# Kernel optimization log

Hardware: AMD Instinct MI355X
Metric: run time of the kernel (lower is better)

## Reference

```python
import jax, jax.numpy as jnp
import numpy as np

NH = 16        # hidden buckets
NG = 32        # static attrs
NR = 16        # routing lags
HS = 256       # MLP hidden size
RHO_WARMUP = 639


def _mlp(x, W1, b1, W2, b2):
    # eval mode: dropout disabled
    return jnp.tanh(x @ W1 + b1) @ W2 + b2


def setup_inputs() -> dict:
    key = jax.random.key(0)
    ks = jax.random.split(key, 16)
    nt, ns = 1000, 500
    x = jax.random.normal(ks[0], (nt, ns, 6), dtype=jnp.float32)
    xc = jax.random.normal(ks[1], (ns, NG), dtype=jnp.float32)

    def lin(k, fan_in, fan_out):
        kw, kb = jax.random.split(k)
        s = 1.0 / np.sqrt(fan_in)
        W = jax.random.uniform(kw, (fan_in, fan_out), jnp.float32, -s, s)
        b = jax.random.uniform(kb, (fan_out,), jnp.float32, -s, s)
        return W, b

    Wr1, br1 = lin(ks[2], NG, HS)
    Wr2, br2 = lin(ks[3], HS, NH * NR)
    Ww1, bw1 = lin(ks[4], NG, HS)
    Ww2, bw2 = lin(ks[5], HS, NH * 7)
    Wt1, bt1 = lin(ks[6], 6 + NG, HS)
    Wt2, bt2 = lin(ks[7], HS, NH * 3)
    return dict(x=x, xc=xc, Wr1=Wr1, br1=br1, Wr2=Wr2, br2=br2,
                Ww1=Ww1, bw1=bw1, Ww2=Ww2, bw2=bw2,
                Wt1=Wt1, bt1=bt1, Wt2=Wt2, bt2=bt2)


def _forward(x, xc, Wr1, br1, Wr2, br2, Ww1, bw1, Ww2, bw2, Wt1, bt1, Wt2, bt2):
    nt, ns, _ = x.shape
    Prcp, Evp, T1, T2 = x[..., 0], x[..., 1], x[..., 2], x[..., 3]

    # ---- static per-basin gate params (wLst activations) ----
    w = _mlp(xc, Ww1, bw1, Ww2, bw2).reshape(ns, NH, 7)
    kp = jax.nn.sigmoid(w[..., 0])   # shallow fast outflow coef
    ksf = jax.nn.sigmoid(w[..., 1])  # shallow slow outflow coef
    kg = jax.nn.sigmoid(w[..., 2])   # deep outflow coef
    gr = jax.nn.sigmoid(w[..., 3])   # recharge fraction
    gL = jnp.exp(w[..., 4])          # shallow capacity
    qb = jax.nn.relu(w[..., 5])      # baseflow
    ga = jax.nn.softmax(w[..., 6], axis=-1)  # bucket mixture ('skip')

    # ---- time-varying params (vLst activations) ----
    xt = jnp.concatenate([x, jnp.broadcast_to(xc[None], (nt, ns, NG))], axis=-1)
    v = _mlp(xt, Wt1, bt1, Wt2, bt2).reshape(nt, ns, NH, 3)
    fi = jax.nn.sigmoid(v[..., 0])             # infiltration fraction
    fm = jax.nn.relu(v[..., 1])                # melt capacity
    Ev = Evp[..., None] * jnp.exp(v[..., 2])   # per-bucket ET

    # ---- divide precipitation into snow / liquid by temperature ----
    vp = jax.nn.sigmoid((T1 + T2) * 0.5)       # [nt, ns]
    Ps = (Prcp * (1.0 - vp))[..., None]        # snow   [nt, ns, 1]
    Pl = (Prcp * vp)[..., None]                # liquid [nt, ns, 1]

    # ---- fused bucket recurrence over time (single scan) ----
    def step(carry, inp):
        Sf, Ss, Sd = carry
        ps, pl, fi_t, fm_t, ev_t = inp
        # snow bucket (long)
        S1 = Sf + ps
        qf = jnp.minimum(S1, fm_t)
        Sf = S1 - qf
        # shallow bucket
        S2 = jax.nn.relu(Ss + pl * fi_t + qf - ev_t)
        qp = jax.nn.relu(S2 - gL) * kp
        qs = jnp.minimum(S2, gL) * ksf
        Ss = S2 - qp - qs
        # deep bucket
        S3 = Sd + qs * gr
        qd = S3 * kg + qb
        Sd = jax.nn.relu(S3 - qd)
        q = qp + qs * (1.0 - gr) + qd
        return (Sf, Ss, Sd), q

    z = jnp.zeros((ns, NH), dtype=x.dtype)
    _, Q = jax.lax.scan(step, (z, z, z), (Ps, Pl, fi, fm, Ev))  # Q: [nt, ns, NH]

    # ---- unit-hydrograph routing over NR lags ----
    r = jax.nn.softmax(_mlp(xc, Wr1, br1, Wr2, br2).reshape(ns, NH, NR), axis=-1)
    Qpad = jnp.pad(Q, ((NR - 1, 0), (0, 0), (0, 0)))
    yR = sum(Qpad[NR - 1 - j: NR - 1 - j + nt] * r[None, :, :, j] for j in range(NR))
    out = jnp.einsum('tsh,sh->ts', yR, ga)
    return out[RHO_WARMUP:]  # [nt - rho_warmup, ns]


def reference(x, xc, Wr1, br1, Wr2, br2, Ww1, bw1, Ww2, bw2, Wt1, bt1, Wt2, bt2):
    return _forward(x, xc, Wr1, br1, Wr2, br2, Ww1, bw1, Ww2, bw2, Wt1, bt1, Wt2, bt2)
```

## Files before the change

### kernel.cpp

```cpp
#include <hip/hip_runtime.h>
#include <hip/hip_fp16.h>

typedef __attribute__((ext_vector_type(8))) _Float16 half8;
typedef __attribute__((ext_vector_type(2))) _Float16 h2v;
typedef __attribute__((ext_vector_type(4))) float f32x4;
typedef __attribute__((ext_vector_type(4))) unsigned short u16x4;
typedef __attribute__((ext_vector_type(2))) unsigned int u32x2;
typedef __attribute__((ext_vector_type(4))) unsigned int u32x4;

#define NTT 1000
#define NSB 500
#define WARM 639

__device__ __forceinline__ float fsig(float x) {
  return __builtin_amdgcn_rcpf(1.f + __expf(-x));
}
__device__ __forceinline__ float ftanh(float x) {
  float e = __expf(-2.f * x);
  return fmaf(2.f, __builtin_amdgcn_rcpf(1.f + e), -1.f);
}
__device__ __forceinline__ float h2f(unsigned short u) {
  __half_raw hr; hr.x = u;
  return __half2float((__half)hr);
}
__device__ __forceinline__ __half2 u2h(unsigned int u) {
  __half2 h; *(unsigned int*)&h = u; return h;
}
__device__ __forceinline__ unsigned int h2u(__half2 h) {
  return *(unsigned int*)&h;
}
__device__ __forceinline__ __half2 hmin2(__half2 a, __half2 b) {
  h2v av = *(h2v*)&a, bv = *(h2v*)&b;
  h2v r = __builtin_elementwise_min(av, bv);
  return *(__half2*)&r;
}

__global__ void prep_bt_kernel(const float* __restrict__ Wt2,
                               const float* __restrict__ Wt1,
                               _Float16* __restrict__ BT,
                               _Float16* __restrict__ W1h) {
  int i = blockIdx.x * 256 + threadIdx.x;
  if (i < 48 * 256) {
    int o = i >> 8, k = i & 255;
    int byte = o * 512 + ((k * 2) ^ ((o & 7) << 4));
    *(_Float16*)((char*)BT + byte) = (_Float16)Wt2[k * 48 + o];
  }
  if (i < 1536) W1h[i] = (_Float16)Wt1[i];
}

__global__ __launch_bounds__(256) void static_kernel(
    const float* __restrict__ xc,
    const float* __restrict__ Wr1, const float* __restrict__ br1,
    const float* __restrict__ Wr2, const float* __restrict__ br2,
    const float* __restrict__ Ww1, const float* __restrict__ bw1,
    const float* __restrict__ Ww2, const float* __restrict__ bw2,
    const float* __restrict__ Wt1, const float* __restrict__ bt1,
    _Float16* __restrict__ c_gh, float* __restrict__ params,
    float* __restrict__ rg)
{
  int s = blockIdx.x, tid = threadIdx.x;
  __shared__ float xcs[32];
  __shared__ float hw[256], hr[256];
  __shared__ float wout[112], rout[256];
  if (tid < 32) xcs[tid] = xc[s * 32 + tid];
  __syncthreads();
  {
    float aw = bw1[tid], ar = br1[tid], ac = bt1[tid];
    #pragma unroll 8
    for (int g = 0; g < 32; ++g) {
      float v = xcs[g];
      aw = fmaf(v, Ww1[g * 256 + tid], aw);
      ar = fmaf(v, Wr1[g * 256 + tid], ar);
      ac = fmaf(v, Wt1[(6 + g) * 256 + tid], ac);
    }
    hw[tid] = ftanh(aw);
    hr[tid] = ftanh(ar);
    c_gh[s * 256 + tid] = (_Float16)ac;
  }
  __syncthreads();
  {
    float acc = br2[tid];
    #pragma unroll 8
    for (int k = 0; k < 256; ++k) acc = fmaf(hr[k], Wr2[k * 256 + tid], acc);
    rout[tid] = acc;
  }
  if (tid < 112) {
    float acc = bw2[tid];
    #pragma unroll 8
    for (int k = 0; k < 256; ++k) acc = fmaf(hw[k], Ww2[k * 112 + tid], acc);
    wout[tid] = acc;
  }
  __syncthreads();
  if (tid < 16) {
    int h = tid;
    float* P = params + (s * 16 + h) * 6;
    P[0] = fsig(wout[h * 7 + 0]);
    P[1] = fsig(wout[h * 7 + 1]);
    P[2] = fsig(wout[h * 7 + 2]);
    P[3] = fsig(wout[h * 7 + 3]);
    P[4] = __expf(wout[h * 7 + 4]);
    P[5] = fmaxf(wout[h * 7 + 5], 0.f);
    float m = -1e30f;
    for (int k = 0; k < 16; ++k) m = fmaxf(m, wout[k * 7 + 6]);
    float den = 0.f;
    for (int k = 0; k < 16; ++k) den += __expf(wout[k * 7 + 6] - m);
    float ga = __expf(wout[h * 7 + 6] - m) * __builtin_amdgcn_rcpf(den);
    float rm = -1e30f;
    for (int j = 0; j < 16; ++j) rm = fmaxf(rm, rout[h * 16 + j]);
    float rden = 0.f;
    for (int j = 0; j < 16; ++j) rden += __expf(rout[h * 16 + j] - rm);
    float sc = ga * __builtin_amdgcn_rcpf(rden);
    for (int j = 0; j < 16; ++j)
      rg[(s * 16 + h) * 16 + j] = __expf(rout[h * 16 + j] - rm) * sc;
  }
}

__global__ __launch_bounds__(256, 5) void tv_kernel(
    const float* __restrict__ x, const _Float16* __restrict__ W1h,
    const float* __restrict__ bt2, const _Float16* __restrict__ c_gh,
    const _Float16* __restrict__ BTg,
    unsigned short* __restrict__ recP)
{
  int s = blockIdx.x;
  int t0 = blockIdx.y * 64;
  int tid = threadIdx.x;
  int w = tid >> 6, l = tid & 63;

  __shared__ _Float16 Abuf[4][16][128];
  __shared__ _Float16 Bbuf[48 * 128];
  __shared__ __half2  xl2[64][8];
  __shared__ float    xe[64][4];

  for (int i = tid; i < 768; i += 256) {
    int o = i >> 4, j = i & 15;
    *(half8*)((char*)Bbuf + o * 256 + j * 16) =
        *(const half8*)((const char*)BTg + o * 512 + j * 16);
  }
  if (tid < 64) {
    int t = t0 + tid;
    float2 a = {0.f, 0.f}, b = a, c = a;
    if (t < NTT) {
      const float* xp = &x[((size_t)t * NSB + s) * 6];
      a = *(const float2*)(xp + 0);
      b = *(const float2*)(xp + 2);
      c = *(const float2*)(xp + 4);
    }
    float vp = fsig(0.5f * (b.x + b.y));
    xe[tid][0] = a.x * vp;
    xe[tid][1] = a.y;
    xe[tid][2] = a.x * (1.f - vp);
    xe[tid][3] = 0.f;
    xl2[tid][0] = __floats2half2_rn(a.x, a.x);
    xl2[tid][1] = __floats2half2_rn(a.y, a.y);
    xl2[tid][2] = __floats2half2_rn(b.x, b.x);
    xl2[tid][3] = __floats2half2_rn(b.y, b.y);
    xl2[tid][4] = __floats2half2_rn(c.x, c.x);
    xl2[tid][5] = __floats2half2_rn(c.y, c.y);
    xl2[tid][6] = __floats2half2_rn(0.f, 0.f);
    xl2[tid][7] = __floats2half2_rn(0.f, 0.f);
  }
  __syncthreads();

  const __half2 one2 = __floats2half2_rn(1.f, 1.f);
  const __half2 mk2  = __floats2half2_rn(-2.88539008f, -2.88539008f);
  const __half2 hi2  = __floats2half2_rn(15.5f, 15.5f);

  __half2 wlo[6], whi[6];
  #pragma unroll
  for (int c = 0; c < 6; ++c) {
    wlo[c] = *(const __half2*)&W1h[c * 256 + 2 * l];
    whi[c] = *(const __half2*)&W1h[c * 256 + 128 + 2 * l];
  }
  __half2 cglo = *(const __half2*)&c_gh[s * 256 + 2 * l];
  __half2 cghi = *(const __half2*)&c_gh[s * 256 + 128 + 2 * l];

  char* aw_base = (char*)&Abuf[w][0][0];
  int col = l & 15, q = l >> 4;
  int arow_xor = (col & 7) << 4;
  const char* Bb = (const char*)Bbuf;
  int r0 = 0 + col, r1 = 16 + col, r2 = 32 + col;
  f32x4 acc0 = {0.f, 0.f, 0.f, 0.f}, acc1 = acc0, acc2 = acc0;

  #pragma unroll
  for (int half = 0; half < 2; ++half) {
    if (half == 1) {
      __syncthreads();
      for (int i = tid; i < 768; i += 256) {
        int o = i >> 4, j = i & 15;
        *(half8*)((char*)Bbuf + o * 256 + j * 16) =
            *(const half8*)((const char*)BTg + o * 512 + 256 + j * 16);
      }
      __syncthreads();
    }
    const __half2* wv = half ? whi : wlo;
    __half2 cg2 = half ? cghi : cglo;
    #pragma unroll
    for (int tt = 0; tt < 16; ++tt) {
      int tr = w * 16 + tt;
      uint4 xa = *(const uint4*)&xl2[tr][0];
      uint2 xb = *(const uint2*)&xl2[tr][4];
      __half2 acc = cg2;
      acc = __hfma2(u2h(xa.x), wv[0], acc);
      acc = __hfma2(u2h(xa.y), wv[1], acc);
      acc = __hfma2(u2h(xa.z), wv[2], acc);
      acc = __hfma2(u2h(xa.w), wv[3], acc);
      acc = __hfma2(u2h(xb.x), wv[4], acc);
      acc = __hfma2(u2h(xb.y), wv[5], acc);
      __half2 t2 = hmin2(__hmul2(acc, mk2), hi2);
      __half2 e = h2exp2(t2);
      __half2 th = __hmul2(__hsub2(one2, e), h2rcp(__hadd2(one2, e)));
      int byte = tt * 256 + ((4 * l) ^ ((tt & 7) << 4));
      *(unsigned int*)(aw_base + byte) = h2u(th);
    }
    #pragma unroll
    for (int ks = 0; ks < 4; ++ks) {
      int kof = ks * 64 + q * 16;
      half8 a  = *(const half8*)(aw_base + col * 256 + (kof ^ arow_xor));
      half8 b0 = *(const half8*)(Bb + r0 * 256 + (kof ^ ((r0 & 7) << 4)));
      half8 b1 = *(const half8*)(Bb + r1 * 256 + (kof ^ ((r1 & 7) << 4)));
      half8 b2 = *(const half8*)(Bb + r2 * 256 + (kof ^ ((r2 & 7) << 4)));
      acc0 = __builtin_amdgcn_mfma_f32_16x16x32_f16(a, b0, acc0, 0, 0, 0);
      acc1 = __builtin_amdgcn_mfma_f32_16x16x32_f16(a, b1, acc1, 0, 0, 0);
      acc2 = __builtin_amdgcn_mfma_f32_16x16x32_f16(a, b2, acc2, 0, 0, 0);
    }
  }

  float b2_0 = bt2[col], b2_1 = bt2[16 + col], b2_2 = bt2[32 + col];
  int c3 = col % 3;
  int ob0 = (3 - c3) % 3;
  int ob1 = (ob0 + 1) % 3;
  int ob2 = (ob0 + 2) % 3;
  int h0 = (16 * ob0 + col) / 3;
  int h1 = (16 * ob1 + col) / 3;
  int h2 = (16 * ob2 + col) / 3;
  #pragma unroll
  for (int i = 0; i < 4; ++i) {
    int tt = q * 4 + i;
    int t = t0 + w * 16 + tt;
    if (t >= NTT) continue;
    float2 pe = *(const float2*)&xe[w * 16 + tt][0];
    float vv0 = acc0[i] + b2_0, vv1 = acc1[i] + b2_1, vv2 = acc2[i] + b2_2;
    float s0 = (ob0 == 0) ? vv0 : (ob0 == 1) ? vv1 : vv2;
    float s1 = (ob1 == 0) ? vv0 : (ob1 == 1) ? vv1 : vv2;
    float s2 = (ob2 == 0) ? vv0 : (ob2 == 1) ? vv1 : vv2;
    char* rowp = aw_base + tt * 128;
    *(__half*)(rowp + h0 * 8 + 0) = __float2half(pe.x * fsig(s0));
    *(__half*)(rowp + h1 * 8 + 2) = __float2half(fmaxf(s1, 0.f));
    *(__half*)(rowp + h2 * 8 + 4) = __float2half(pe.y * __expf(s2));
  }
  #pragma unroll
  for (int k2 = 0; k2 < 4; ++k2) {
    int idx = k2 * 64 + l;
    int tt = idx >> 4, h = idx & 15;
    int t = t0 + w * 16 + tt;
    if (t < NTT) {
      u16x4 r4 = *(const u16x4*)(aw_base + tt * 128 + h * 8);
      __half psh = __float2half(xe[w * 16 + tt][2]);
      r4[3] = *(unsigned short*)&psh;
      *(u16x4*)&recP[((size_t)t * 8000 + s * 16 + h) * 4] = r4;
    }
  }
}

struct Rec8 { u32x2 r[8]; };

__device__ __forceinline__ void issue8(Rec8& c, int tb, int tid,
                                       const char* recP)
{
  #pragma unroll
  for (int u = 0; u < 8; ++u) {
    int t = tb + u; t = t < NTT ? t : NTT - 1;
    unsigned long long addr =
        (unsigned long long)(recP + ((size_t)t * 8000 + tid) * 8);
    asm volatile("global_load_dwordx2 %0, %1, off"
                 : "=v"(c.r[u]) : "v"(addr));
  }
}

__device__ __forceinline__ void comp8(
    const Rec8& c, int tb, u32x4* Qlds4, int lane,
    float& Sf, float& Ss, float& Sd,
    float kp, float ksf, float kg, float gr, float gL, float qb, float omgr)
{
  float qv[8];
  #pragma unroll
  for (int u = 0; u < 8; ++u) {
    float pli = h2f((unsigned short)(c.r[u].x & 0xffff));
    float fm  = h2f((unsigned short)(c.r[u].x >> 16));
    float ev  = h2f((unsigned short)(c.r[u].y & 0xffff));
    float ps  = h2f((unsigned short)(c.r[u].y >> 16));
    float ce  = pli - ev;
    float S1 = Sf + ps;
    float qf = fminf(S1, fm);
    Sf = S1 - qf;
    float S2 = fmaxf((Ss + ce) + qf, 0.f);
    float qp = fmaxf(S2 - gL, 0.f) * kp;
    float qs = fminf(S2, gL) * ksf;
    Ss = S2 - qp - qs;
    float S3 = fmaf(qs, gr, Sd);
    float qd = fmaf(S3, kg, qb);
    Sd = fmaxf(S3 - qd, 0.f);
    qv[u] = fmaf(qs, omgr, qp) + qd;
  }
  if (tb < NTT) {
    u32x4 q4;
    q4.x = h2u(__floats2half2_rn(qv[0], qv[1]));
    q4.y = h2u(__floats2half2_rn(qv[2], qv[3]));
    q4.z = h2u(__floats2half2_rn(qv[4], qv[5]));
    q4.w = h2u(__floats2half2_rn(qv[6], qv[7]));
    Qlds4[(tb >> 3) * 64 + lane] = q4;
  }
}

#define SCAN_PHASE(CK, OFF) \
  asm volatile("s_waitcnt vmcnt(40)" ::: "memory"); \
  __builtin_amdgcn_sched_barrier(0); \
  comp8(CK, tb + OFF, Qlds4, lane, Sf, Ss, Sd, kp, ksf, kg, gr, gL, qb, omgr); \
  issue8(CK, tb + 48 + OFF, tid, rb); \
  __builtin_amdgcn_sched_barrier(0);

__global__ __launch_bounds__(64, 1) void scan_kernel(
    const float* __restrict__ params,
    const unsigned short* __restrict__ recP,
    __half* __restrict__ Qg2)
{
  __shared__ u32x4 Qlds4[125 * 64];
  int lane = threadIdx.x;
  int tid = blockIdx.x * 64 + lane;
  const float* P = params + tid * 6;
  float kp = P[0], ksf = P[1], kg = P[2], gr = P[3], gL = P[4], qb = P[5];
  float omgr = 1.f - gr;
  asm volatile("" : "+v"(kp), "+v"(ksf), "+v"(kg), "+v"(gr), "+v"(gL));
  asm volatile("" : "+v"(qb), "+v"(omgr));
  asm volatile("s_waitcnt vmcnt(0)" ::: "memory");
  __builtin_amdgcn_sched_barrier(0);

  float Sf = 0.f, Ss = 0.f, Sd = 0.f;
  const char* rb = (const char*)recP;

  Rec8 C0, C1, C2, C3, C4, C5;
  issue8(C0,  0, tid, rb);
  issue8(C1,  8, tid, rb);
  issue8(C2, 16, tid, rb);
  issue8(C3, 24, tid, rb);
  issue8(C4, 32, tid, rb);
  issue8(C5, 40, tid, rb);
  __builtin_amdgcn_sched_barrier(0);
  for (int i = 0; i < 21; ++i) {
    int tb = i * 48;
    SCAN_PHASE(C0,  0)
    SCAN_PHASE(C1,  8)
    SCAN_PHASE(C2, 16)
    SCAN_PHASE(C3, 24)
    SCAN_PHASE(C4, 32)
    SCAN_PHASE(C5, 40)
  }
  asm volatile("s_waitcnt vmcnt(0)" ::: "memory");
  __builtin_amdgcn_sched_barrier(0);
  size_t gbase = (size_t)tid * 1024;
  for (int k = 0; k < 125; ++k) {
    u32x4 v = Qlds4[k * 64 + lane];
    *(u32x4*)(Qg2 + gbase + k * 8) = v;
  }
}

__global__ __launch_bounds__(128) void route_kernel(
    const __half* __restrict__ Qg2, const float* __restrict__ rg,
    float* __restrict__ out)
{
  int s = blockIdx.x;
  int t0 = WARM + blockIdx.y * 128;
  int tid = threadIdx.x;
  __shared__ float Qs[16][144];
  __shared__ float rgs[16][16];
  {
    int h = tid & 15, c = tid >> 4;
    const __half* src = Qg2 + (size_t)(s * 16 + h) * 1024 + (t0 - 15);
    #pragma unroll
    for (int cc = 0; cc < 3; ++cc) {
      int ch = c + cc * 8;
      if (ch < 18) {
        half8 v8 = *(const half8*)(src + ch * 8);
        #pragma unroll
        for (int j = 0; j < 8; ++j) {
          int idx = ch * 8 + j;
          if (idx < 143) Qs[h][idx] = (float)v8[j];
        }
      }
    }
  }
  for (int i = tid; i < 256; i += 128) {
    int h = i >> 4, j = i & 15;
    rgs[j][h] = rg[s * 256 + i];
  }
  __syncthreads();
  int t = t0 + tid;
  if (t < NTT) {
    float acc = 0.f;
    #pragma unroll
    for (int j = 0; j < 16; ++j) {
      int row = tid + 15 - j;
      #pragma unroll
      for (int h = 0; h < 16; ++h)
        acc = fmaf(Qs[h][row], rgs[j][h], acc);
    }
    out[(t - WARM) * NSB + s] = acc;
  }
}

extern "C" void kernel_launch(void* const* d_in, const int* in_sizes, int n_in,
                              void* d_out, int out_size, void* d_ws, size_t ws_size,
                              hipStream_t stream)
{
  const float* x   = (const float*)d_in[0];
  const float* xc  = (const float*)d_in[1];
  const float* Wr1 = (const float*)d_in[2];
  const float* br1 = (const float*)d_in[3];
  const float* Wr2 = (const float*)d_in[4];
  const float* br2 = (const float*)d_in[5];
  const float* Ww1 = (const float*)d_in[6];
  const float* bw1 = (const float*)d_in[7];
  const float* Ww2 = (const float*)d_in[8];
  const float* bw2 = (const float*)d_in[9];
  const float* Wt1 = (const float*)d_in[10];
  const float* bt1 = (const float*)d_in[11];
  const float* Wt2 = (const float*)d_in[12];
  const float* bt2 = (const float*)d_in[13];

  char* w = (char*)d_ws;
  unsigned short* recP = (unsigned short*)(w);
  __half* Qg2   = (__half*)(w + 64000000);
  float*  params= (float*)(w + 80384000);
  float*  rgw   = (float*)(w + 80576000);
  _Float16* BT  = (_Float16*)(w + 81088000);
  _Float16* W1h = (_Float16*)(w + 81112576);
  _Float16* c_gh= (_Float16*)(w + 81115648);

  prep_bt_kernel<<<48, 256, 0, stream>>>(Wt2, Wt1, BT, W1h);
  static_kernel<<<500, 256, 0, stream>>>(xc, Wr1, br1, Wr2, br2,
                                         Ww1, bw1, Ww2, bw2, Wt1, bt1,
                                         c_gh, params, rgw);
  tv_kernel<<<dim3(500, 16), 256, 0, stream>>>(x, W1h, bt2, c_gh, BT, recP);
  scan_kernel<<<125, 64, 0, stream>>>(params, recP, Qg2);
  route_kernel<<<dim3(500, 3), 128, 0, stream>>>(Qg2, rgw, (float*)d_out);
}
```

Before: 171.8 us.

## Fold tanh into sigmoid via prescaled weights and merge prep kernel

Rewrites the hidden tanh as 2*sigmoid(2x)-1, prescaling W1 and the static hidden bias by -2*log2(e) and folding the W2 column sums into a new bias. This trims fp16 ops in the hot hidden-activation loop of tv_kernel. Also merges the weight-prep kernel into static_kernel to drop a launch, simplifies scan load addressing using an SGPR base without clamping, and pads an LDS array. The unclamped scan loads read past the last time row into the workspace, and the changed fp16 formulation slightly alters numerics.

```diff
diff --git a/kernel.cpp b/kernel.cpp
--- a/kernel.cpp
+++ b/kernel.cpp
@@ -11,6 +11,7 @@
 #define NTT 1000
 #define NSB 500
 #define WARM 639
+#define MKF (-2.8853900817779268f)
 
 __device__ __forceinline__ float fsig(float x) {
   return __builtin_amdgcn_rcpf(1.f + __expf(-x));
@@ -33,19 +34,6 @@
   h2v av = *(h2v*)&a, bv = *(h2v*)&b;
   h2v r = __builtin_elementwise_min(av, bv);
   return *(__half2*)&r;
-}
-
-__global__ void prep_bt_kernel(const float* __restrict__ Wt2,
-                               const float* __restrict__ Wt1,
-                               _Float16* __restrict__ BT,
-                               _Float16* __restrict__ W1h) {
-  int i = blockIdx.x * 256 + threadIdx.x;
-  if (i < 48 * 256) {
-    int o = i >> 8, k = i & 255;
-    int byte = o * 512 + ((k * 2) ^ ((o & 7) << 4));
-    *(_Float16*)((char*)BT + byte) = (_Float16)Wt2[k * 48 + o];
-  }
-  if (i < 1536) W1h[i] = (_Float16)Wt1[i];
 }
 
 __global__ __launch_bounds__(256) void static_kernel(
@@ -55,8 +43,11 @@
     const float* __restrict__ Ww1, const float* __restrict__ bw1,
     const float* __restrict__ Ww2, const float* __restrict__ bw2,
     const float* __restrict__ Wt1, const float* __restrict__ bt1,
+    const float* __restrict__ Wt2, const float* __restrict__ bt2,
     _Float16* __restrict__ c_gh, float* __restrict__ params,
-    float* __restrict__ rg)
+    float* __restrict__ rg,
+    _Float16* __restrict__ BT, _Float16* __restrict__ W1h,
+    float* __restrict__ bS)
 {
   int s = blockIdx.x, tid = threadIdx.x;
   __shared__ float xcs[32];
@@ -75,7 +66,7 @@
     }
     hw[tid] = ftanh(aw);
     hr[tid] = ftanh(ar);
-    c_gh[s * 256 + tid] = (_Float16)ac;
+    c_gh[s * 256 + tid] = (_Float16)(ac * MKF);
   }
   __syncthreads();
   {
@@ -113,11 +104,26 @@
     for (int j = 0; j < 16; ++j)
       rg[(s * 16 + h) * 16 + j] = __expf(rout[h * 16 + j] - rm) * sc;
   }
+  if (s < 48) {
+    int o = s, k = tid;
+    float w2v = Wt2[k * 48 + o];
+    int byte = o * 512 + ((k * 2) ^ ((o & 7) << 4));
+    *(_Float16*)((char*)BT + byte) = (_Float16)w2v;
+    if (s < 6) W1h[s * 256 + tid] = (_Float16)(Wt1[s * 256 + tid] * MKF);
+    __syncthreads();
+    hw[tid] = w2v;
+    __syncthreads();
+    for (int st = 128; st > 0; st >>= 1) {
+      if (tid < st) hw[tid] += hw[tid + st];
+      __syncthreads();
+    }
+    if (tid == 0) bS[o] = bt2[o] - hw[0];
+  }
 }
 
 __global__ __launch_bounds__(256, 5) void tv_kernel(
     const float* __restrict__ x, const _Float16* __restrict__ W1h,
-    const float* __restrict__ bt2, const _Float16* __restrict__ c_gh,
+    const float* __restrict__ bS, const _Float16* __restrict__ c_gh,
     const _Float16* __restrict__ BTg,
     unsigned short* __restrict__ recP)
 {
@@ -162,7 +168,6 @@
   __syncthreads();
 
   const __half2 one2 = __floats2half2_rn(1.f, 1.f);
-  const __half2 mk2  = __floats2half2_rn(-2.88539008f, -2.88539008f);
   const __half2 hi2  = __floats2half2_rn(15.5f, 15.5f);
 
   __half2 wlo[6], whi[6];
@@ -206,11 +211,10 @@
       acc = __hfma2(u2h(xa.w), wv[3], acc);
       acc = __hfma2(u2h(xb.x), wv[4], acc);
       acc = __hfma2(u2h(xb.y), wv[5], acc);
-      __half2 t2 = hmin2(__hmul2(acc, mk2), hi2);
-      __half2 e = h2exp2(t2);
-      __half2 th = __hmul2(__hsub2(one2, e), h2rcp(__hadd2(one2, e)));
+      __half2 e = h2exp2(hmin2(acc, hi2));
+      __half2 sg = h2rcp(__hadd2(one2, e));
       int byte = tt * 256 + ((4 * l) ^ ((tt & 7) << 4));
-      *(unsigned int*)(aw_base + byte) = h2u(th);
+      *(unsigned int*)(aw_base + byte) = h2u(sg);
     }
     #pragma unroll
     for (int ks = 0; ks < 4; ++ks) {
@@ -225,7 +229,7 @@
     }
   }
 
-  float b2_0 = bt2[col], b2_1 = bt2[16 + col], b2_2 = bt2[32 + col];
+  float bs0 = bS[col], bs1 = bS[16 + col], bs2 = bS[32 + col];
   int c3 = col % 3;
   int ob0 = (3 - c3) % 3;
   int ob1 = (ob0 + 1) % 3;
@@ -239,7 +243,9 @@
     int t = t0 + w * 16 + tt;
     if (t >= NTT) continue;
     float2 pe = *(const float2*)&xe[w * 16 + tt][0];
-    float vv0 = acc0[i] + b2_0, vv1 = acc1[i] + b2_1, vv2 = acc2[i] + b2_2;
+    float vv0 = fmaf(2.f, acc0[i], bs0);
+    float vv1 = fmaf(2.f, acc1[i], bs1);
+    float vv2 = fmaf(2.f, acc2[i], bs2);
     float s0 = (ob0 == 0) ? vv0 : (ob0 == 1) ? vv1 : vv2;
     float s1 = (ob1 == 0) ? vv0 : (ob1 == 1) ? vv1 : vv2;
     float s2 = (ob2 == 0) ? vv0 : (ob2 == 1) ? vv1 : vv2;
@@ -264,16 +270,14 @@
 
 struct Rec8 { u32x2 r[8]; };
 
-__device__ __forceinline__ void issue8(Rec8& c, int tb, int tid,
+__device__ __forceinline__ void issue8(Rec8& c, int tB, unsigned voff,
                                        const char* recP)
 {
   #pragma unroll
   for (int u = 0; u < 8; ++u) {
-    int t = tb + u; t = t < NTT ? t : NTT - 1;
-    unsigned long long addr =
-        (unsigned long long)(recP + ((size_t)t * 8000 + tid) * 8);
-    asm volatile("global_load_dwordx2 %0, %1, off"
-                 : "=v"(c.r[u]) : "v"(addr));
+    const char* base = recP + (size_t)(tB + u) * 64000;
+    asm volatile("global_load_dwordx2 %0, %1, %2 offset:0"
+                 : "=v"(c.r[u]) : "v"(voff), "s"(base));
   }
 }
 
@@ -316,7 +320,7 @@
   asm volatile("s_waitcnt vmcnt(40)" ::: "memory"); \
   __builtin_amdgcn_sched_barrier(0); \
   comp8(CK, tb + OFF, Qlds4, lane, Sf, Ss, Sd, kp, ksf, kg, gr, gL, qb, omgr); \
-  issue8(CK, tb + 48 + OFF, tid, rb); \
+  issue8(CK, tb + 48 + OFF, voff, rb); \
   __builtin_amdgcn_sched_barrier(0);
 
 __global__ __launch_bounds__(64, 1) void scan_kernel(
@@ -327,6 +331,7 @@
   __shared__ u32x4 Qlds4[125 * 64];
   int lane = threadIdx.x;
   int tid = blockIdx.x * 64 + lane;
+  unsigned voff = (unsigned)tid * 8;
   const float* P = params + tid * 6;
   float kp = P[0], ksf = P[1], kg = P[2], gr = P[3], gL = P[4], qb = P[5];
   float omgr = 1.f - gr;
@@ -339,12 +344,12 @@
   const char* rb = (const char*)recP;
 
   Rec8 C0, C1, C2, C3, C4, C5;
-  issue8(C0,  0, tid, rb);
-  issue8(C1,  8, tid, rb);
-  issue8(C2, 16, tid, rb);
-  issue8(C3, 24, tid, rb);
-  issue8(C4, 32, tid, rb);
-  issue8(C5, 40, tid, rb);
+  issue8(C0,  0, voff, rb);
+  issue8(C1,  8, voff, rb);
+  issue8(C2, 16, voff, rb);
+  issue8(C3, 24, voff, rb);
+  issue8(C4, 32, voff, rb);
+  issue8(C5, 40, voff, rb);
   __builtin_amdgcn_sched_barrier(0);
   for (int i = 0; i < 21; ++i) {
     int tb = i * 48;
@@ -371,7 +376,7 @@
   int s = blockIdx.x;
   int t0 = WARM + blockIdx.y * 128;
   int tid = threadIdx.x;
-  __shared__ float Qs[16][144];
+  __shared__ float Qs[16][145];
   __shared__ float rgs[16][16];
   {
     int h = tid & 15, c = tid >> 4;
@@ -435,12 +440,13 @@
   _Float16* BT  = (_Float16*)(w + 81088000);
   _Float16* W1h = (_Float16*)(w + 81112576);
   _Float16* c_gh= (_Float16*)(w + 81115648);
-
-  prep_bt_kernel<<<48, 256, 0, stream>>>(Wt2, Wt1, BT, W1h);
+  float*  bS    = (float*)(w + 81371648);
+
   static_kernel<<<500, 256, 0, stream>>>(xc, Wr1, br1, Wr2, br2,
                                          Ww1, bw1, Ww2, bw2, Wt1, bt1,
-                                         c_gh, params, rgw);
-  tv_kernel<<<dim3(500, 16), 256, 0, stream>>>(x, W1h, bt2, c_gh, BT, recP);
+                                         Wt2, bt2,
+                                         c_gh, params, rgw, BT, W1h, bS);
+  tv_kernel<<<dim3(500, 16), 256, 0, stream>>>(x, W1h, bS, c_gh, BT, recP);
   scan_kernel<<<125, 64, 0, stream>>>(params, recP, Qg2);
   route_kernel<<<dim3(500, 3), 128, 0, stream>>>(Qg2, rgw, (float*)d_out);
 }
```

Measured after the change: 158.6 us. -7.6%, faster.
